# Optimization experiments

Hardware: AMD Instinct MI355X
Metric: run time of the kernel (lower is better)

Reference implementation:

```python
import jax, jax.numpy as jnp
import numpy as np

D_MODEL, HEADS, D_K = 512, 8, 64
MIN_SPREAD, MIN_RBF, MAX_RBF = 2.0, 0.001, 1.0
NEG_INF = float('-inf')


def setup_inputs() -> dict:
    key = jax.random.key(0)
    ks = jax.random.split(key, 12)
    B, N = 2, 2048
    xav = (6.0 / (D_K + D_MODEL)) ** 0.5
    unif = lambda k, shape: jax.random.uniform(k, shape, jnp.float32, -xav, xav)
    return {
        'q': jax.random.normal(ks[0], (B, N, D_MODEL), jnp.float32),
        'k': jax.random.normal(ks[1], (B, N, D_MODEL), jnp.float32),
        'v': jax.random.normal(ks[2], (B, N, D_MODEL), jnp.float32),
        'coords': jax.random.normal(ks[3], (B, N, 3), jnp.float32),
        'mask': jnp.zeros((B, N), dtype=bool),
        'spread_weights': jnp.zeros((HEADS,), jnp.float32),
        'beta_weights': jnp.zeros((HEADS,), jnp.float32),
        'q_proj': unif(ks[4], (HEADS, D_MODEL, D_K)),
        'k_proj': unif(ks[5], (HEADS, D_MODEL, D_K)),
        'v_proj': unif(ks[6], (HEADS, D_MODEL, D_K)),
        'q_bias': jnp.zeros((HEADS, D_K), jnp.float32),
        'k_bias': jnp.zeros((HEADS, D_K), jnp.float32),
        'v_bias': jnp.zeros((HEADS, D_K), jnp.float32),
        'w_out': jax.random.normal(ks[7], (D_MODEL, D_MODEL), jnp.float32) * (1.0 / D_MODEL ** 0.5),
    }


def reference(q, k, v, coords, mask, spread_weights, beta_weights,
              q_proj, k_proj, v_proj, q_bias, k_bias, v_bias, w_out):
    B, N, _ = q.shape
    # per-head projections: [B,H,N,dk]
    Q = jnp.einsum('bnd,hdk->bhnk', q, q_proj) + q_bias[None, :, None, :]
    K = jnp.einsum('bnd,hdk->bhnk', k, k_proj) + k_bias[None, :, None, :]
    V = jnp.einsum('bnd,hdk->bhnk', v, v_proj) + v_bias[None, :, None, :]
    # scaled dot-product scores [B,H,N,N]
    S = jnp.einsum('bhnk,bhmk->bhnm', Q, K) / (D_K ** 0.5)
    # squared pairwise distances [B,N,N] (D = sqrt(D2); RBF uses -D^2 = -D2)
    D2 = jnp.sum((coords[:, :, None, :] - coords[:, None, :, :]) ** 2, axis=-1)
    spreads = MIN_SPREAD + jnp.exp(spread_weights)  # [H]
    betas = jnp.exp(beta_weights)                   # [H]
    R = jnp.exp(-D2[:, None, :, :] / (2.0 * spreads[None, :, None, None] ** 2))
    R_norm = 2.0 * (R - MIN_RBF) / (MAX_RBF - MIN_RBF) - 1.0
    SR = S + jnp.abs(S) * betas[None, :, None, None] * R_norm
    SR = jnp.where(mask[:, None, None, :], NEG_INF, SR)  # eval mode: drop_p = 0
    P = jax.nn.softmax(SR, axis=-1)
    out = jnp.einsum('bhnm,bhmk->bhnk', P, V)  # [B,H,N,dk]
    # permute(0,2,3,1) -> [B,N,dk,H], reshape to [B,N,d_model]
    out = jnp.transpose(out, (0, 2, 3, 1)).reshape(B, N, D_MODEL)
    return out @ w_out.T
```

## Files before the change

kernel.cpp:

```cpp
#include <hip/hip_runtime.h>
#include <hip/hip_fp16.h>

typedef unsigned short u16;
typedef unsigned int u32;
typedef __attribute__((ext_vector_type(4))) float f32x4;
typedef __attribute__((ext_vector_type(8))) short s16x8;
typedef __attribute__((ext_vector_type(2))) unsigned int u32x2;
typedef __fp16 fp16x2 __attribute__((ext_vector_type(2)));

#define B_SZ 2
#define N_SZ 2048
#define H_SZ 8
#define DK 64
#define DM 512
#define QSC 0.18033688f

static __device__ inline void mfma_f16(f32x4& acc, s16x8 a, s16x8 b) {
    asm volatile("v_mfma_f32_16x16x32_f16 %0, %1, %2, %0" : "+v"(acc) : "v"(a), "v"(b));
}
static __device__ inline u16 f16_rn(float f) { return __half_as_ushort(__float2half(f)); }

static __device__ inline u32 pkrtz(float a, float b) {
    union { fp16x2 h; u32 u; } cv;
    cv.h = __builtin_amdgcn_cvt_pkrtz(a, b);
    return cv.u;
}

#if __has_builtin(__builtin_amdgcn_exp2f)
#define EXP2(x) __builtin_amdgcn_exp2f(x)
#else
#define EXP2(x) exp2f(x)
#endif

static __device__ inline s16x8 cvt8(const float4& a, const float4& b) {
    s16x8 r;
    r[0] = (short)f16_rn(a.x); r[1] = (short)f16_rn(a.y);
    r[2] = (short)f16_rn(a.z); r[3] = (short)f16_rn(a.w);
    r[4] = (short)f16_rn(b.x); r[5] = (short)f16_rn(b.y);
    r[6] = (short)f16_rn(b.z); r[7] = (short)f16_rn(b.w);
    return r;
}

static __device__ inline u16* swz(u16* base, int row, int byteoff) {
    return (u16*)((char*)base + row * 128 + (byteoff ^ ((row & 7) << 4)));
}
static __device__ inline const u16* swzc(const u16* base, int row, int byteoff) {
    return (const u16*)((const char*)base + row * 128 + (byteoff ^ ((row & 7) << 4)));
}

#if __has_builtin(__builtin_amdgcn_global_load_lds)
#define HAS_GLL 1
static __device__ inline void gll16(const u16* g, u16* l) {
    __builtin_amdgcn_global_load_lds(
        (const __attribute__((address_space(1))) unsigned int*)g,
        (__attribute__((address_space(3))) unsigned int*)l, 16, 0, 0);
}
#endif
static __device__ inline void stage16(const u16* gp, u16* lbase, int lane) {
#ifdef HAS_GLL
    gll16(gp, lbase);
#else
    *(s16x8*)(lbase + lane * 8) = *(const s16x8*)(gp);
#endif
}

static __device__ inline void stage_tile_swz(const u16* tile, u16* lds, int wl, int lane) {
#pragma unroll
    for (int c = 0; c < 2; c++) {
        int Lb = c * 4096 + wl * 1024 + lane * 16;
        int row = Lb >> 7, off = Lb & 127;
        const u16* src = tile + row * 64 + (((off ^ ((row & 7) << 4))) >> 1);
        u16* dst = (u16*)((char*)lds + c * 4096 + wl * 1024);
#ifdef HAS_GLL
        gll16(src, dst);
#else
        *(s16x8*)((char*)dst + lane * 16) = *(const s16x8*)src;
#endif
    }
}

__global__ void __launch_bounds__(256) k_prep(
    const float* __restrict__ q, const float* __restrict__ k,
    const float* __restrict__ v, const float* __restrict__ qp,
    const float* __restrict__ kp, const float* __restrict__ vp,
    const float* __restrict__ wo, const float* __restrict__ coords,
    const unsigned char* __restrict__ maskp,
    u16* __restrict__ Pt, u16* __restrict__ Wb2, u16* __restrict__ Af,
    float4* __restrict__ C4, float* __restrict__ mbias) {
    int blk = blockIdx.x, t = threadIdx.x;
    __shared__ float lds[64 * 65];
    if (blk < 192) {
        int z = blk >> 6, rem = blk & 63, h = rem >> 3, ddt = rem & 7;
        const float* src = (z == 0 ? qp : (z == 1 ? kp : vp)) + (size_t)h * DM * DK;
        u16* dst = Pt + ((size_t)(z * H_SZ + h)) * DK * DM;
        float sc = (z == 0) ? QSC : 1.0f;
#pragma unroll
        for (int i = 0; i < 16; i++) {
            int idx = i * 256 + t;
            int rr = idx >> 6, cc = idx & 63;
            lds[cc * 65 + rr] = src[(size_t)(ddt * 64 + rr) * DK + cc];
        }
        __syncthreads();
#pragma unroll
        for (int i = 0; i < 16; i++) {
            int idx = i * 256 + t;
            int kk = idx >> 6, dd = idx & 63;
            dst[(size_t)kk * DM + ddt * 64 + dd] = f16_rn(lds[kk * 65 + dd] * sc);
        }
    } else if (blk < 320) {
        int idx8 = (blk - 192) * 256 + t;
        int base = idx8 * 8;
        int c = base >> 9, col0 = base & 511;
        int h = col0 >> 6, d0 = col0 & 63;
        s16x8 r;
#pragma unroll
        for (int i = 0; i < 8; i++)
            r[i] = (short)f16_rn(wo[(size_t)c * 512 + (d0 + i) * 8 + h]);
        *(s16x8*)(Wb2 + base) = r;
    } else if (blk < 3392) {
        size_t base = (size_t)(blk - 320) * 2048 + (size_t)t * 8;
        int z = (int)(base >> 21);
        size_t off = base & 2097151;
        const float* s = (z == 0 ? q : (z == 1 ? k : v)) + off;
        float4 f0 = *(const float4*)(s);
        float4 f1 = *(const float4*)(s + 4);
        *(s16x8*)(Af + base) = cvt8(f0, f1);
    } else {
        int i = (blk - 3392) * 256 + t;
        float x = coords[(size_t)i * 3], y = coords[(size_t)i * 3 + 1], z = coords[(size_t)i * 3 + 2];
        C4[i] = make_float4(x, y, z, x * x + y * y + z * z);
        mbias[i] = maskp[i] ? -1e30f : 0.0f;
    }
}

__global__ void __launch_bounds__(256) k_proj_gemm(
    const u16* __restrict__ Af, const u16* __restrict__ Pt,
    const float* __restrict__ qbias, const float* __restrict__ kbias,
    const float* __restrict__ vbias,
    u16* __restrict__ Qb, u16* __restrict__ Kb, u16* __restrict__ Vt) {
    int bid = blockIdx.x;
    int wid = (bid & 7) * 96 + (bid >> 3);
    int c0 = (wid & 7) * 64;
    int zm = wid >> 3;
    int m0 = (zm & 31) * 128;
    int z = zm >> 5;
    const u16* A = Af + (size_t)z * (4096 * 512);
    const float* bias = z == 0 ? qbias : (z == 1 ? kbias : vbias);
    const u16* Bw = Pt + (size_t)z * (512 * 512);
    int t = threadIdx.x, w = t >> 6, l = t & 63, g = (l >> 4), cl = l & 15;
    __shared__ __align__(16) u16 a_lds[2][128 * 64];
    f32x4 acc[2][4] = {};
    int srow_b = w * 8 + (l >> 3), schk = l & 7;

#define STAGE_P(ks, buf)                                                              \
    {                                                                                 \
        _Pragma("unroll") for (int cc = 0; cc < 4; cc++) {                            \
            int row = cc * 32 + srow_b;                                               \
            const u16* gp = A + (size_t)(m0 + row) * 512 + (ks) * 64 +                \
                            ((schk ^ (row & 7)) << 3);                                \
            stage16(gp, a_lds[buf] + cc * 2048 + w * 512, l);                         \
        }                                                                             \
    }

    STAGE_P(0, 0);
    for (int ks = 0; ks < 8; ks++) {
        int cur = ks & 1;
        __syncthreads();
        if (ks < 7) STAGE_P(ks + 1, cur ^ 1);
        s16x8 bfrag[4][2];
#pragma unroll
        for (int st = 0; st < 4; st++) {
            int c = c0 + st * 16 + cl;
#pragma unroll
            for (int kk = 0; kk < 2; kk++)
                bfrag[st][kk] = *(const s16x8*)(Bw + (size_t)c * 512 + ks * 64 + kk * 32 + 8 * g);
        }
#pragma unroll
        for (int rs = 0; rs < 2; rs++) {
            int row = w * 32 + rs * 16 + cl;
#pragma unroll
            for (int kk = 0; kk < 2; kk++) {
                s16x8 afrag = *(const s16x8*)swzc(a_lds[cur], row, kk * 64 + 16 * g);
#pragma unroll
                for (int st = 0; st < 4; st++) mfma_f16(acc[rs][st], afrag, bfrag[st][kk]);
            }
        }
    }
#undef STAGE_P

    if (z == 2) {
        int h = c0 >> 6;
        int b = m0 >> 11;
        u16* vl = a_lds[0];
        __syncthreads();
#pragma unroll
        for (int rs = 0; rs < 2; rs++) {
#pragma unroll
            for (int st = 0; st < 4; st++) {
                int d = st * 16 + cl;
                float bv = bias[c0 + st * 16 + cl];
#pragma unroll
                for (int r = 0; r < 4; r++) {
                    int row = w * 32 + rs * 16 + 4 * g + r;
                    int jt = row >> 6, jl = row & 63;
                    int jp = (jl & 15) * 4 + (jl >> 4);
                    vl[jt * 4096 + d * 64 + jp] = f16_rn(acc[rs][st][r] + bv);
                }
            }
        }
        __syncthreads();
        int jt = t >> 7, rem = t & 127, d = rem >> 1, qh = t & 1;
        const u16* src = vl + jt * 4096 + d * 64 + qh * 32;
        int jtile = ((m0 & 2047) >> 6) + jt;
        u16* dst = Vt + ((size_t)((b * H_SZ + h) * 32 + jtile)) * 4096 + d * 64 + qh * 32;
        *(s16x8*)(dst) = *(const s16x8*)(src);
        *(s16x8*)(dst + 8) = *(const s16x8*)(src + 8);
        *(s16x8*)(dst + 16) = *(const s16x8*)(src + 16);
        *(s16x8*)(dst + 24) = *(const s16x8*)(src + 24);
    } else {
        float bsc = (z == 0) ? QSC : 1.0f;
        u16* dst = (z == 0) ? Qb : Kb;
#pragma unroll
        for (int rs = 0; rs < 2; rs++) {
#pragma unroll
            for (int st = 0; st < 4; st++) {
                int c = c0 + st * 16 + cl;
                int h = c >> 6, kk = c & 63;
                float bv = bias[c] * bsc;
#pragma unroll
                for (int r = 0; r < 4; r++) {
                    int m = m0 + w * 32 + rs * 16 + 4 * g + r;
                    int b = m >> 11, n = m & 2047;
                    dst[((size_t)(b * H_SZ + h) * N_SZ + n) * DK + kk] = f16_rn(acc[rs][st][r] + bv);
                }
            }
        }
    }
}

__global__ void __launch_bounds__(512, 4) k_attn(
    const u16* __restrict__ Qb, const u16* __restrict__ Kb,
    const u16* __restrict__ Vt, const float4* __restrict__ C4,
    const float* __restrict__ mbias,
    const float* __restrict__ spread_w, const float* __restrict__ beta_w,
    u16* __restrict__ Om) {
    int bid = blockIdx.x;
    int wid = (bid & 7) * 64 + (bid >> 3);
    int qt = wid & 31, bh = wid >> 5;
    int h = bh & 7, b = bh >> 3;
    int n0 = qt * 64;
    int t = threadIdx.x, w = t >> 6, l = t & 63, g = l >> 4, cl = l & 15;
    int wq = w & 3, half = w >> 2;

    __shared__ __align__(16) u16 kbuf[2][2][4096];
    __shared__ __align__(16) u16 vbuf[2][2][4096];
    __shared__ __align__(16) u16 pbuf[8][1024];

    const u16* qp = Qb + ((size_t)bh * N_SZ + n0 + wq * 16 + cl) * DK;
    s16x8 qf0 = *(const s16x8*)(qp + 8 * g);
    s16x8 qf1 = *(const s16x8*)(qp + 32 + 8 * g);

    float sigma = 2.0f + __expf(spread_w[h]);
    float ninv2 = -0.72134752f / (sigma * sigma);
    float beta = __expf(beta_w[h]);
    float rnA = 2.002002f * beta, rnB = -1.002002f * beta;
    float m2n = -2.0f * ninv2;

    float qx2[4], qy2[4], qz2[4], aR[4];
#pragma unroll
    for (int r = 0; r < 4; r++) {
        float4 c4 = C4[b * N_SZ + n0 + wq * 16 + 4 * g + r];
        qx2[r] = c4.x * m2n; qy2[r] = c4.y * m2n; qz2[r] = c4.z * m2n;
        aR[r] = ninv2 * c4.w;
    }

    float mrun[4] = {-1e30f, -1e30f, -1e30f, -1e30f};
    float lsum[4] = {0.f, 0.f, 0.f, 0.f};
    f32x4 oacc[4] = {};

    const u16* kbase = Kb + (size_t)bh * N_SZ * DK;
    const u16* vbase = Vt + (size_t)bh * 32 * 4096;
    const float4* c4b = C4 + b * N_SZ;
    const float* mbb = mbias + b * N_SZ;

    stage_tile_swz(kbase + (size_t)(half * 64) * 64, &kbuf[0][half][0], wq, l);
    stage_tile_swz(vbase + (size_t)half * 4096,      &vbuf[0][half][0], wq, l);

    for (int it = 0; it < 16; it++) {
        int cur = it & 1;
        int jt = it * 2 + half, j0 = jt * 64;
        __syncthreads();
        if (it < 15) {
            int jn = jt + 2;
            stage_tile_swz(kbase + (size_t)(jn * 64) * 64, &kbuf[cur ^ 1][half][0], wq, l);
            stage_tile_swz(vbase + (size_t)jn * 4096,      &vbuf[cur ^ 1][half][0], wq, l);
        }
        float4 ccv[4]; float mbv[4];
#pragma unroll
        for (int st = 0; st < 4; st++) {
            ccv[st] = c4b[j0 + st * 16 + cl];
            mbv[st] = mbb[j0 + st * 16 + cl];
        }
        f32x4 s[4];
#pragma unroll
        for (int st = 0; st < 4; st++) {
            int jj = st * 16 + cl;
            s16x8 kf0 = *(const s16x8*)swzc(&kbuf[cur][half][0], jj, 16 * g);
            s16x8 kf1 = *(const s16x8*)swzc(&kbuf[cur][half][0], jj, 64 + 16 * g);
            f32x4 a = {};
            mfma_f16(a, qf0, kf0);
            mfma_f16(a, qf1, kf1);
            s[st] = a;
        }
        float sr[4][4];
#pragma unroll
        for (int st = 0; st < 4; st++) {
            float bJ = ninv2 * ccv[st].w;
#pragma unroll
            for (int r = 0; r < 4; r++) {
                float arg = fmaf(qx2[r], ccv[st].x,
                            fmaf(qy2[r], ccv[st].y,
                            fmaf(qz2[r], ccv[st].z, aR[r] + bJ)));
                float rb = EXP2(arg);
                float sv = s[st][r];
                sr[st][r] = fmaf(fabsf(sv), fmaf(rnA, rb, rnB), sv) + mbv[st];
            }
        }
        float tmx[4]; bool need = false;
#pragma unroll
        for (int r = 0; r < 4; r++) {
            float tm = fmaxf(fmaxf(sr[0][r], sr[1][r]), fmaxf(sr[2][r], sr[3][r]));
            tm = fmaxf(tm, __shfl_xor(tm, 1));
            tm = fmaxf(tm, __shfl_xor(tm, 2));
            tm = fmaxf(tm, __shfl_xor(tm, 4));
            tm = fmaxf(tm, __shfl_xor(tm, 8));
            tmx[r] = tm;
            need = need || (tm > mrun[r] + 8.0f);
        }
        if (__any(need)) {
#pragma unroll
            for (int r = 0; r < 4; r++) {
                float mn = fmaxf(mrun[r], tmx[r]);
                float corr = EXP2(mrun[r] - mn);
                mrun[r] = mn;
                lsum[r] *= corr;
#pragma unroll
                for (int dst = 0; dst < 4; dst++) oacc[dst][r] *= corr;
            }
        }
#pragma unroll
        for (int r = 0; r < 4; r++) {
            float p0 = EXP2(sr[0][r] - mrun[r]);
            float p1 = EXP2(sr[1][r] - mrun[r]);
            float p2 = EXP2(sr[2][r] - mrun[r]);
            float p3 = EXP2(sr[3][r] - mrun[r]);
            lsum[r] += (p0 + p1) + (p2 + p3);
            u32x2 pw = {pkrtz(p0, p1), pkrtz(p2, p3)};
            *(u32x2*)swz(pbuf[w], 4 * g + r, cl * 8) = pw;
        }
#pragma unroll
        for (int ks = 0; ks < 2; ks++) {
            s16x8 pf = *(const s16x8*)swzc(pbuf[w], cl, ks * 64 + 16 * g);
#pragma unroll
            for (int dst = 0; dst < 4; dst++) {
                s16x8 vf = *(const s16x8*)swzc(&vbuf[cur][half][0], dst * 16 + cl, ks * 64 + 16 * g);
                mfma_f16(oacc[dst], pf, vf);
            }
        }
    }
#pragma unroll
    for (int r = 0; r < 4; r++) {
        float s = lsum[r];
        s += __shfl_xor(s, 1); s += __shfl_xor(s, 2);
        s += __shfl_xor(s, 4); s += __shfl_xor(s, 8);
        lsum[r] = s;
    }
    __syncthreads();
    float* scrO = (float*)(&kbuf[0][0][0]);
    float* scrM = (float*)(&vbuf[0][0][0]);
    if (half == 1) {
#pragma unroll
        for (int r = 0; r < 4; r++) {
            int rr = 4 * g + r;
#pragma unroll
            for (int dst = 0; dst < 4; dst++)
                scrO[wq * 1024 + rr * 64 + dst * 16 + cl] = oacc[dst][r];
            if (cl == 0) {
                scrM[wq * 32 + rr] = mrun[r];
                scrM[wq * 32 + 16 + rr] = lsum[r];
            }
        }
    }
    __syncthreads();
    if (half == 0) {
#pragma unroll
        for (int r = 0; r < 4; r++) {
            int rr = 4 * g + r;
            float mu = scrM[wq * 32 + rr], lu = scrM[wq * 32 + 16 + rr];
            float M = fmaxf(mrun[r], mu);
            float pa = EXP2(mrun[r] - M), pb = EXP2(mu - M);
            float inv = 1.0f / (pa * lsum[r] + pb * lu);
            int row = n0 + wq * 16 + rr;
#pragma unroll
            for (int dst = 0; dst < 4; dst++) {
                float o = (pa * oacc[dst][r] + pb * scrO[wq * 1024 + rr * 64 + dst * 16 + cl]) * inv;
                Om[((size_t)b * N_SZ + row) * DM + h * 64 + dst * 16 + cl] = f16_rn(o);
            }
        }
    }
}

__global__ void __launch_bounds__(256) k_out_gemm(
    const u16* __restrict__ Om, const u16* __restrict__ Wb2,
    float* __restrict__ out) {
    int bid = blockIdx.x;
    int wid = (bid & 7) * 32 + (bid >> 3);
    int c0 = (wid & 7) * 64;
    int m0 = (wid >> 3) * 128;
    int t = threadIdx.x, w = t >> 6, l = t & 63, g = (l >> 4), cl = l & 15;
    __shared__ __align__(16) u16 a_lds[2][128 * 64];
    f32x4 acc[2][4] = {};
    int srow_b = w * 8 + (l >> 3), schk = l & 7;

#define STAGE_O(ks, buf)                                                              \
    {                                                                                 \
        _Pragma("unroll") for (int cc = 0; cc < 4; cc++) {                            \
            int row = cc * 32 + srow_b;                                               \
            const u16* gp = Om + (size_t)(m0 + row) * 512 + (ks) * 64 +               \
                            ((schk ^ (row & 7)) << 3);                                \
            stage16(gp, a_lds[buf] + cc * 2048 + w * 512, l);                         \
        }                                                                             \
    }

    STAGE_O(0, 0);
    for (int ks = 0; ks < 8; ks++) {
        int cur = ks & 1;
        __syncthreads();
        if (ks < 7) STAGE_O(ks + 1, cur ^ 1);
        s16x8 bfrag[4][2];
#pragma unroll
        for (int st = 0; st < 4; st++) {
            int c = c0 + st * 16 + cl;
#pragma unroll
            for (int kk = 0; kk < 2; kk++)
                bfrag[st][kk] = *(const s16x8*)(Wb2 + (size_t)c * 512 + ks * 64 + kk * 32 + 8 * g);
        }
#pragma unroll
        for (int rs = 0; rs < 2; rs++) {
            int row = w * 32 + rs * 16 + cl;
#pragma unroll
            for (int kk = 0; kk < 2; kk++) {
                s16x8 afrag = *(const s16x8*)swzc(a_lds[cur], row, kk * 64 + 16 * g);
#pragma unroll
                for (int st = 0; st < 4; st++) mfma_f16(acc[rs][st], afrag, bfrag[st][kk]);
            }
        }
    }
#undef STAGE_O
#pragma unroll
    for (int rs = 0; rs < 2; rs++) {
#pragma unroll
        for (int st = 0; st < 4; st++) {
            int c = c0 + st * 16 + cl;
#pragma unroll
            for (int r = 0; r < 4; r++) {
                int m = m0 + w * 32 + rs * 16 + 4 * g + r;
                out[(size_t)m * 512 + c] = acc[rs][st][r];
            }
        }
    }
}

extern "C" void kernel_launch(void* const* d_in, const int* in_sizes, int n_in,
                              void* d_out, int out_size, void* d_ws, size_t ws_size,
                              hipStream_t stream) {
    const float* q      = (const float*)d_in[0];
    const float* k      = (const float*)d_in[1];
    const float* v      = (const float*)d_in[2];
    const float* coords = (const float*)d_in[3];
    const unsigned char* mask = (const unsigned char*)d_in[4];
    const float* sw     = (const float*)d_in[5];
    const float* bw     = (const float*)d_in[6];
    const float* qp     = (const float*)d_in[7];
    const float* kp     = (const float*)d_in[8];
    const float* vp     = (const float*)d_in[9];
    const float* qbias  = (const float*)d_in[10];
    const float* kbias  = (const float*)d_in[11];
    const float* vbias  = (const float*)d_in[12];
    const float* wo     = (const float*)d_in[13];

    char* ws = (char*)d_ws;
    u16*    Pt    = (u16*)(ws);
    u16*    Wb2   = (u16*)(ws + 1572864);
    u16*    Af    = (u16*)(ws + 2097152);
    u16*    Qb    = (u16*)(ws + 14680064);
    u16*    Kb    = (u16*)(ws + 18874368);
    u16*    Vt    = (u16*)(ws + 23068672);
    u16*    Om    = (u16*)(ws + 27262976);
    float4* C4    = (float4*)(ws + 31457280);
    float*  mbias = (float*)(ws + 31522816);

    k_prep<<<dim3(3408), 256, 0, stream>>>(q, k, v, qp, kp, vp, wo, coords, mask,
                                           Pt, Wb2, Af, C4, mbias);
    k_proj_gemm<<<dim3(768), 256, 0, stream>>>(Af, Pt, qbias, kbias, vbias, Qb, Kb, Vt);
    k_attn<<<dim3(512), 512, 0, stream>>>(Qb, Kb, Vt, C4, mbias, sw, bw, Om);
    k_out_gemm<<<dim3(256), 256, 0, stream>>>(Om, Wb2, (float*)d_out);
}
```

Baseline: 203.0 us.

## Fuse fp32-to-fp16 activation conversion into projection GEMM and add MFMA priority hints

The separate prep pass that converted q/k/v activations to fp16 in a workspace buffer is removed. The projection GEMM now loads fp32 tiles straight into registers, converts them with packed round-toward-zero and writes them to a single swizzled LDS buffer, prefetching the next tile in registers. This drops a full write and re-read of the converted activations. In exchange the GEMM gains an extra barrier per k-step and uses round-toward-zero instead of round-to-nearest. The attention kernel also raises wave priority with s_setprio around its MFMA blocks.

```diff
diff --git a/kernel.cpp b/kernel.cpp
--- a/kernel.cpp
+++ b/kernel.cpp
@@ -31,15 +31,6 @@
 #else
 #define EXP2(x) exp2f(x)
 #endif
-
-static __device__ inline s16x8 cvt8(const float4& a, const float4& b) {
-    s16x8 r;
-    r[0] = (short)f16_rn(a.x); r[1] = (short)f16_rn(a.y);
-    r[2] = (short)f16_rn(a.z); r[3] = (short)f16_rn(a.w);
-    r[4] = (short)f16_rn(b.x); r[5] = (short)f16_rn(b.y);
-    r[6] = (short)f16_rn(b.z); r[7] = (short)f16_rn(b.w);
-    return r;
-}
 
 static __device__ inline u16* swz(u16* base, int row, int byteoff) {
     return (u16*)((char*)base + row * 128 + (byteoff ^ ((row & 7) << 4)));
@@ -80,12 +71,10 @@
 }
 
 __global__ void __launch_bounds__(256) k_prep(
-    const float* __restrict__ q, const float* __restrict__ k,
-    const float* __restrict__ v, const float* __restrict__ qp,
-    const float* __restrict__ kp, const float* __restrict__ vp,
-    const float* __restrict__ wo, const float* __restrict__ coords,
-    const unsigned char* __restrict__ maskp,
-    u16* __restrict__ Pt, u16* __restrict__ Wb2, u16* __restrict__ Af,
+    const float* __restrict__ qp, const float* __restrict__ kp,
+    const float* __restrict__ vp, const float* __restrict__ wo,
+    const float* __restrict__ coords, const unsigned char* __restrict__ maskp,
+    u16* __restrict__ Pt, u16* __restrict__ Wb2,
     float4* __restrict__ C4, float* __restrict__ mbias) {
     int blk = blockIdx.x, t = threadIdx.x;
     __shared__ float lds[64 * 65];
@@ -117,16 +106,8 @@
         for (int i = 0; i < 8; i++)
             r[i] = (short)f16_rn(wo[(size_t)c * 512 + (d0 + i) * 8 + h]);
         *(s16x8*)(Wb2 + base) = r;
-    } else if (blk < 3392) {
-        size_t base = (size_t)(blk - 320) * 2048 + (size_t)t * 8;
-        int z = (int)(base >> 21);
-        size_t off = base & 2097151;
-        const float* s = (z == 0 ? q : (z == 1 ? k : v)) + off;
-        float4 f0 = *(const float4*)(s);
-        float4 f1 = *(const float4*)(s + 4);
-        *(s16x8*)(Af + base) = cvt8(f0, f1);
     } else {
-        int i = (blk - 3392) * 256 + t;
+        int i = (blk - 320) * 256 + t;
         float x = coords[(size_t)i * 3], y = coords[(size_t)i * 3 + 1], z = coords[(size_t)i * 3 + 2];
         C4[i] = make_float4(x, y, z, x * x + y * y + z * z);
         mbias[i] = maskp[i] ? -1e30f : 0.0f;
@@ -134,7 +115,8 @@
 }
 
 __global__ void __launch_bounds__(256) k_proj_gemm(
-    const u16* __restrict__ Af, const u16* __restrict__ Pt,
+    const float* __restrict__ q, const float* __restrict__ k,
+    const float* __restrict__ v, const u16* __restrict__ Pt,
     const float* __restrict__ qbias, const float* __restrict__ kbias,
     const float* __restrict__ vbias,
     u16* __restrict__ Qb, u16* __restrict__ Kb, u16* __restrict__ Vt) {
@@ -144,29 +126,37 @@
     int zm = wid >> 3;
     int m0 = (zm & 31) * 128;
     int z = zm >> 5;
-    const u16* A = Af + (size_t)z * (4096 * 512);
+    const float* A = z == 0 ? q : (z == 1 ? k : v);
     const float* bias = z == 0 ? qbias : (z == 1 ? kbias : vbias);
     const u16* Bw = Pt + (size_t)z * (512 * 512);
     int t = threadIdx.x, w = t >> 6, l = t & 63, g = (l >> 4), cl = l & 15;
-    __shared__ __align__(16) u16 a_lds[2][128 * 64];
+    __shared__ __align__(16) u16 a_lds[128 * 64];
     f32x4 acc[2][4] = {};
-    int srow_b = w * 8 + (l >> 3), schk = l & 7;
-
-#define STAGE_P(ks, buf)                                                              \
+    int sr16 = t >> 4, sc16 = t & 15;
+
+    float4 f[8];
+#define LOADA(ks)                                                                     \
     {                                                                                 \
-        _Pragma("unroll") for (int cc = 0; cc < 4; cc++) {                            \
-            int row = cc * 32 + srow_b;                                               \
-            const u16* gp = A + (size_t)(m0 + row) * 512 + (ks) * 64 +                \
-                            ((schk ^ (row & 7)) << 3);                                \
-            stage16(gp, a_lds[buf] + cc * 2048 + w * 512, l);                         \
+        _Pragma("unroll") for (int i = 0; i < 8; i++) {                               \
+            int row = i * 16 + sr16;                                                  \
+            f[i] = *(const float4*)(A + (size_t)(m0 + row) * 512 + (ks) * 64 + sc16 * 4); \
         }                                                                             \
     }
-
-    STAGE_P(0, 0);
+#define WRITEA()                                                                      \
+    {                                                                                 \
+        _Pragma("unroll") for (int i = 0; i < 8; i++) {                               \
+            int row = i * 16 + sr16;                                                  \
+            u32x2 pw = {pkrtz(f[i].x, f[i].y), pkrtz(f[i].z, f[i].w)};                \
+            *(u32x2*)swz(a_lds, row, sc16 * 8) = pw;                                  \
+        }                                                                             \
+    }
+
+    LOADA(0);
     for (int ks = 0; ks < 8; ks++) {
-        int cur = ks & 1;
-        __syncthreads();
-        if (ks < 7) STAGE_P(ks + 1, cur ^ 1);
+        __syncthreads();
+        WRITEA();
+        if (ks < 7) LOADA(ks + 1);
+        __syncthreads();
         s16x8 bfrag[4][2];
 #pragma unroll
         for (int st = 0; st < 4; st++) {
@@ -180,18 +170,19 @@
             int row = w * 32 + rs * 16 + cl;
 #pragma unroll
             for (int kk = 0; kk < 2; kk++) {
-                s16x8 afrag = *(const s16x8*)swzc(a_lds[cur], row, kk * 64 + 16 * g);
+                s16x8 afrag = *(const s16x8*)swzc(a_lds, row, kk * 64 + 16 * g);
 #pragma unroll
                 for (int st = 0; st < 4; st++) mfma_f16(acc[rs][st], afrag, bfrag[st][kk]);
             }
         }
     }
-#undef STAGE_P
+#undef LOADA
+#undef WRITEA
 
     if (z == 2) {
         int h = c0 >> 6;
         int b = m0 >> 11;
-        u16* vl = a_lds[0];
+        u16* vl = a_lds;
         __syncthreads();
 #pragma unroll
         for (int rs = 0; rs < 2; rs++) {
@@ -302,6 +293,7 @@
             mbv[st] = mbb[j0 + st * 16 + cl];
         }
         f32x4 s[4];
+        __builtin_amdgcn_s_setprio(1);
 #pragma unroll
         for (int st = 0; st < 4; st++) {
             int jj = st * 16 + cl;
@@ -312,6 +304,7 @@
             mfma_f16(a, qf1, kf1);
             s[st] = a;
         }
+        __builtin_amdgcn_s_setprio(0);
         float sr[4][4];
 #pragma unroll
         for (int st = 0; st < 4; st++) {
@@ -358,6 +351,7 @@
             u32x2 pw = {pkrtz(p0, p1), pkrtz(p2, p3)};
             *(u32x2*)swz(pbuf[w], 4 * g + r, cl * 8) = pw;
         }
+        __builtin_amdgcn_s_setprio(1);
 #pragma unroll
         for (int ks = 0; ks < 2; ks++) {
             s16x8 pf = *(const s16x8*)swzc(pbuf[w], cl, ks * 64 + 16 * g);
@@ -367,6 +361,7 @@
                 mfma_f16(oacc[dst], pf, vf);
             }
         }
+        __builtin_amdgcn_s_setprio(0);
     }
 #pragma unroll
     for (int r = 0; r < 4; r++) {
@@ -492,17 +487,16 @@
     char* ws = (char*)d_ws;
     u16*    Pt    = (u16*)(ws);
     u16*    Wb2   = (u16*)(ws + 1572864);
-    u16*    Af    = (u16*)(ws + 2097152);
-    u16*    Qb    = (u16*)(ws + 14680064);
-    u16*    Kb    = (u16*)(ws + 18874368);
-    u16*    Vt    = (u16*)(ws + 23068672);
-    u16*    Om    = (u16*)(ws + 27262976);
-    float4* C4    = (float4*)(ws + 31457280);
-    float*  mbias = (float*)(ws + 31522816);
-
-    k_prep<<<dim3(3408), 256, 0, stream>>>(q, k, v, qp, kp, vp, wo, coords, mask,
-                                           Pt, Wb2, Af, C4, mbias);
-    k_proj_gemm<<<dim3(768), 256, 0, stream>>>(Af, Pt, qbias, kbias, vbias, Qb, Kb, Vt);
+    u16*    Qb    = (u16*)(ws + 2097152);
+    u16*    Kb    = (u16*)(ws + 6291456);
+    u16*    Vt    = (u16*)(ws + 10485760);
+    u16*    Om    = (u16*)(ws + 14680064);
+    float4* C4    = (float4*)(ws + 18874368);
+    float*  mbias = (float*)(ws + 18939904);
+
+    k_prep<<<dim3(336), 256, 0, stream>>>(qp, kp, vp, wo, coords, mask,
+                                          Pt, Wb2, C4, mbias);
+    k_proj_gemm<<<dim3(768), 256, 0, stream>>>(q, k, v, Pt, qbias, kbias, vbias, Qb, Kb, Vt);
     k_attn<<<dim3(512), 512, 0, stream>>>(Qb, Kb, Vt, C4, mbias, sw, bw, Om);
     k_out_gemm<<<dim3(256), 256, 0, stream>>>(Om, Wb2, (float*)d_out);
 }
```

New measurement: 200.7 us. Within noise of the previous version (-1.1%).
